# Optimization experiments

Measured on AMD Instinct MI355X. Metric: run time of the kernel, lower is better.

## Reference

```python
import jax, jax.numpy as jnp
import numpy as np

HEADS = 4
DIM_HEAD = 32
DIM = 128
EPS = 1e-12  # F.normalize eps


def _rmsnorm(t, g):
    # F.normalize over channel dim (dim=1), then * g * sqrt(dim)
    n = jnp.sqrt(jnp.sum(t * t, axis=1, keepdims=True))
    return t / jnp.maximum(n, EPS) * g * (DIM ** 0.5)


def setup_inputs() -> dict:
    key = jax.random.key(0)
    ks = jax.random.split(key, 5)
    b, H, W = 16, 96, 96
    x = jax.random.normal(ks[0], (b, DIM, H, W), dtype=jnp.float32)
    norm_g = jnp.ones((1, DIM, 1, 1), dtype=jnp.float32)
    qkv_w = jax.random.normal(ks[1], (3 * HEADS * DIM_HEAD, DIM), dtype=jnp.float32) * 0.05
    mem_kv = jax.random.normal(ks[2], (2, HEADS, DIM_HEAD, 4), dtype=jnp.float32)
    out_w = jax.random.normal(ks[3], (DIM, HEADS * DIM_HEAD), dtype=jnp.float32) * 0.05
    out_b = jnp.zeros((DIM,), dtype=jnp.float32)
    out_norm_g = jnp.ones((1, DIM, 1, 1), dtype=jnp.float32)
    return {"x": x, "norm_g": norm_g, "qkv_w": qkv_w, "mem_kv": mem_kv,
            "out_w": out_w, "out_b": out_b, "out_norm_g": out_norm_g}


def reference(x, norm_g, qkv_w, mem_kv, out_w, out_b, out_norm_g):
    b, c, H, W = x.shape
    n = H * W
    scale = DIM_HEAD ** (-0.5)

    xn = _rmsnorm(x, norm_g)
    # 1x1 conv (no bias) == channel GEMM
    qkv = jnp.einsum('oc,bchw->bohw', qkv_w, xn)  # [b, 3*h*d, H, W]
    q, k, v = jnp.split(qkv, 3, axis=1)

    def to_heads(t):
        return t.reshape(b, HEADS, DIM_HEAD, n)  # b h d n

    q, k, v = to_heads(q), to_heads(k), to_heads(v)

    mk = jnp.broadcast_to(mem_kv[0], (b, HEADS, DIM_HEAD, mem_kv.shape[-1]))
    mv = jnp.broadcast_to(mem_kv[1], (b, HEADS, DIM_HEAD, mem_kv.shape[-1]))
    k = jnp.concatenate([mk, k], axis=-1)
    v = jnp.concatenate([mv, v], axis=-1)

    q = jax.nn.softmax(q, axis=-2) * scale  # softmax over d
    k = jax.nn.softmax(k, axis=-1)          # softmax over n

    context = jnp.einsum('bhdn,bhen->bhde', k, v)  # [b,h,d,d]
    out = jnp.einsum('bhde,bhdn->bhen', context, q)  # [b,h,d,n]
    out = out.reshape(b, HEADS * DIM_HEAD, H, W)

    out = jnp.einsum('oc,bchw->bohw', out_w, out) + out_b[None, :, None, None]
    return _rmsnorm(out, out_norm_g)
```

## Files before the change

kernel.cpp:

```cpp
#include <hip/hip_runtime.h>
#include <hip/hip_bf16.h>
#include <math.h>

#define NPIX 9216
#define NBLK 48
#define TPB 6
#define NTILE 288
#define SCALE 0.17677669529663687f
#define SQRT128 11.313708498984761f

typedef __attribute__((ext_vector_type(8))) short short8;
typedef __attribute__((ext_vector_type(4))) float f32x4;

static __device__ __forceinline__ unsigned short f2bf(float f) {
  return __bfloat16_as_ushort(__float2bfloat16(f));
}
static __device__ __forceinline__ float bf2f(unsigned short h) {
  return __bfloat162float(__ushort_as_bfloat16(h));
}


__global__ __launch_bounds__(256) void k_prep2(
    const float* __restrict__ qkv_w, const float* __restrict__ norm_g,
    const float* __restrict__ out_w,
    unsigned short* __restrict__ wbf2, unsigned short* __restrict__ owb2) {
  const int i = blockIdx.x * 256 + threadIdx.x;
  if (i < 6144) {
    const int g = i >> 6, lane = i & 63;
    const int wv = g / 24, rem = g % 24;
    const int mt = rem >> 2, ks = rem & 3;
    const int row = 96 * wv + mt * 16 + (lane & 15);
    const int col = ks * 32 + (lane >> 4) * 8;
    const float* src = qkv_w + row * 128 + col;
    const float* gg = norm_g + col;
    uint4 o;
    o.x = (unsigned)f2bf(src[0] * gg[0]) | ((unsigned)f2bf(src[1] * gg[1]) << 16);
    o.y = (unsigned)f2bf(src[2] * gg[2]) | ((unsigned)f2bf(src[3] * gg[3]) << 16);
    o.z = (unsigned)f2bf(src[4] * gg[4]) | ((unsigned)f2bf(src[5] * gg[5]) << 16);
    o.w = (unsigned)f2bf(src[6] * gg[6]) | ((unsigned)f2bf(src[7] * gg[7]) << 16);
    *(uint4*)(wbf2 + (size_t)i * 8) = o;
  } else if (i < 8192) {
    const int i2 = i - 6144;
    const int g = i2 >> 6, lane = i2 & 63;
    const int wv = g >> 3, rem = g & 7;
    const int mt = rem >> 2, ks = rem & 3;
    const int row = 32 * wv + mt * 16 + (lane & 15);
    const int col = ks * 32 + (lane >> 4) * 8;
    const float* src = out_w + row * 128 + col;
    uint4 o;
    o.x = (unsigned)f2bf(src[0]) | ((unsigned)f2bf(src[1]) << 16);
    o.y = (unsigned)f2bf(src[2]) | ((unsigned)f2bf(src[3]) << 16);
    o.z = (unsigned)f2bf(src[4]) | ((unsigned)f2bf(src[5]) << 16);
    o.w = (unsigned)f2bf(src[6]) | ((unsigned)f2bf(src[7]) << 16);
    *(uint4*)(owb2 + (size_t)i2 * 8) = o;
  }
}

__global__ __launch_bounds__(256) void k_init(const float* __restrict__ mem_kv,
                                              float* __restrict__ ctxG,
                                              float* __restrict__ sumexpG) {
  const int bh = blockIdx.x;
  const int h = bh & 3;
  const float* mk = mem_kv + h * 128;
  const float* mv = mem_kv + 512 + h * 128;
  const int t = threadIdx.x;
  const int d = t >> 3, e0 = (t & 7) * 4;
  float ek[4], se = 0.f;
#pragma unroll
  for (int j = 0; j < 4; ++j) { ek[j] = __expf(mk[d * 4 + j]); se += ek[j]; }
#pragma unroll
  for (int ei = 0; ei < 4; ++ei) {
    const int e = e0 + ei;
    float s = 0.f;
#pragma unroll
    for (int j = 0; j < 4; ++j) s += ek[j] * mv[e * 4 + j];
    ctxG[(bh * 32 + d) * 32 + e] = s;
  }
  if ((t & 7) == 0) sumexpG[bh * 32 + d] = se;
}

template <bool WSQ>
__global__ __launch_bounds__(256, 2) void k1(
    const float* __restrict__ x, const unsigned short* __restrict__ wbf2,
    unsigned short* __restrict__ qb16, float* __restrict__ qf32,
    float* __restrict__ ctx_dst, float* __restrict__ se_dst) {
  __shared__ __align__(16) unsigned char smem[30720 + 8704 + 4096 + 128];
  unsigned short* qkv = (unsigned short*)smem;
  unsigned short* xnT = (unsigned short*)(smem + 30720);
  float* redu = (float*)(smem + 30720 + 8704);
  float* inv = (float*)(smem + 30720 + 8704 + 4096);

  const int t = threadIdx.x;
  const int b = blockIdx.y;
  const int blk = blockIdx.x;
  const int wv = t >> 6;
  const int lane = t & 63;
  const int lr = lane & 15;
  const int lg = lane >> 4;
  const int r = t >> 3, c4 = (t & 7) * 4;
  const float* xb = x + ((size_t)b * 128) * NPIX + blk * TPB * 32;

  f32x4 acc[6][2];
  f32x4 ctx[2][2];
#pragma unroll
  for (int i = 0; i < 6; ++i)
#pragma unroll
    for (int j = 0; j < 2; ++j)
#pragma unroll
      for (int q = 0; q < 4; ++q) acc[i][j][q] = 0.f;
#pragma unroll
  for (int i = 0; i < 2; ++i)
#pragma unroll
    for (int j = 0; j < 2; ++j)
#pragma unroll
      for (int q = 0; q < 4; ++q) ctx[i][j][q] = 0.f;
  float se_row[2] = {0.f, 0.f};

  float4 pf[4];
#pragma unroll
  for (int pass = 0; pass < 4; ++pass)
    pf[pass] = *(const float4*)(xb + (size_t)(pass * 32 + r) * NPIX + c4);

  for (int it = 0; it < TPB; ++it) {
    const int tile = blk * TPB + it;

    {
      float ss0 = 0.f, ss1 = 0.f, ss2 = 0.f, ss3 = 0.f;
#pragma unroll
      for (int pass = 0; pass < 4; ++pass) {
        const int row = pass * 32 + r;
        const float4 v = pf[pass];
        xnT[(c4 + 0) * 136 + row] = f2bf(v.x);
        xnT[(c4 + 1) * 136 + row] = f2bf(v.y);
        xnT[(c4 + 2) * 136 + row] = f2bf(v.z);
        xnT[(c4 + 3) * 136 + row] = f2bf(v.w);
        ss0 = fmaf(v.x, v.x, ss0); ss1 = fmaf(v.y, v.y, ss1);
        ss2 = fmaf(v.z, v.z, ss2); ss3 = fmaf(v.w, v.w, ss3);
      }
      *(float4*)&redu[r * 32 + c4] = make_float4(ss0, ss1, ss2, ss3);
    }
    __syncthreads();
    {
      short8 bfr[4][2];
#pragma unroll
      for (int ks = 0; ks < 4; ++ks)
#pragma unroll
        for (int nt = 0; nt < 2; ++nt)
          bfr[ks][nt] = *(const short8*)&xnT[(nt * 16 + lr) * 136 + ks * 32 + lg * 8];
      if (it + 1 < TPB) {
        const float* xb2 = xb + (it + 1) * 32;
#pragma unroll
        for (int pass = 0; pass < 4; ++pass)
          pf[pass] = *(const float4*)(xb2 + (size_t)(pass * 32 + r) * NPIX + c4);
      }
      if (t < 32) {
        float s = 0.f;
#pragma unroll
        for (int g = 0; g < 32; ++g) s += redu[g * 32 + t];
        inv[t] = SQRT128 / fmaxf(sqrtf(s), 1e-12f);
      }
      const unsigned short* wbase = wbf2 + (size_t)(wv * 24) * 512 + lane * 8;
#pragma unroll
      for (int mt = 0; mt < 6; ++mt) {
#pragma unroll
        for (int ks = 0; ks < 4; ++ks) {
          const short8 af = *(const short8*)(wbase + (size_t)(mt * 4 + ks) * 512);
          acc[mt][0] = __builtin_amdgcn_mfma_f32_16x16x32_bf16(af, bfr[ks][0], acc[mt][0], 0, 0, 0);
          acc[mt][1] = __builtin_amdgcn_mfma_f32_16x16x32_bf16(af, bfr[ks][1], acc[mt][1], 0, 0, 0);
        }
      }
    }
    __syncthreads();
    {
      const float iv0 = inv[lr], iv1 = inv[16 + lr];
#pragma unroll
      for (int mt = 0; mt < 6; ++mt)
#pragma unroll
        for (int nt = 0; nt < 2; ++nt) {
          const float iv = nt ? iv1 : iv0;
#pragma unroll
          for (int q = 0; q < 4; ++q) {
            const int row = 96 * wv + mt * 16 + lg * 4 + q;
            qkv[row * 40 + nt * 16 + lr] = f2bf(acc[mt][nt][q] * iv);
            acc[mt][nt][q] = 0.f;
          }
        }
    }
    __syncthreads();
    {
      const int c0 = wv * 32 + lg * 8;
#pragma unroll
      for (int px = 0; px < 2; ++px) {
        const int p = px * 16 + lr;
        float qv[8];
#pragma unroll
        for (int j = 0; j < 8; ++j) qv[j] = bf2f(qkv[(c0 + j) * 40 + p]);
        float m = qv[0];
#pragma unroll
        for (int j = 1; j < 8; ++j) m = fmaxf(m, qv[j]);
        m = fmaxf(m, __shfl_xor(m, 16));
        m = fmaxf(m, __shfl_xor(m, 32));
        float s = 0.f;
#pragma unroll
        for (int j = 0; j < 8; ++j) { qv[j] = __expf(qv[j] - m); s += qv[j]; }
        s += __shfl_xor(s, 16);
        s += __shfl_xor(s, 32);
        const float rs = SCALE / s;
        if (WSQ) {
          uint4 qo;
          qo.x = (unsigned)f2bf(qv[0] * rs) | ((unsigned)f2bf(qv[1] * rs) << 16);
          qo.y = (unsigned)f2bf(qv[2] * rs) | ((unsigned)f2bf(qv[3] * rs) << 16);
          qo.z = (unsigned)f2bf(qv[4] * rs) | ((unsigned)f2bf(qv[5] * rs) << 16);
          qo.w = (unsigned)f2bf(qv[6] * rs) | ((unsigned)f2bf(qv[7] * rs) << 16);
          *(uint4*)(qb16 +
              ((((size_t)(b * NTILE + tile) * 4 + wv) * 2 + px) * 64 + lane) * 8) = qo;
        } else {
#pragma unroll
          for (int j = 0; j < 8; ++j)
            qf32[((size_t)b * 128 + c0 + j) * NPIX + tile * 32 + p] = qv[j] * rs;
        }
      }
      short8 afk[2];
#pragma unroll
      for (int dt = 0; dt < 2; ++dt) {
        const short8 kraw = *(const short8*)&qkv[(128 + wv * 32 + dt * 16 + lr) * 40 + lg * 8];
        short8 e16;
        float s = 0.f;
#pragma unroll
        for (int j = 0; j < 8; ++j) {
          const float ev = __expf(bf2f((unsigned short)kraw[j]));
          e16[j] = (short)f2bf(ev);
          s += ev;
        }
        afk[dt] = e16;
        s += __shfl_xor(s, 16);
        s += __shfl_xor(s, 32);
        se_row[dt] += s;
      }
#pragma unroll
      for (int dt = 0; dt < 2; ++dt)
#pragma unroll
        for (int et = 0; et < 2; ++et) {
          const short8 bf = *(const short8*)&qkv[(256 + wv * 32 + et * 16 + lr) * 40 + lg * 8];
          ctx[dt][et] = __builtin_amdgcn_mfma_f32_16x16x32_bf16(afk[dt], bf, ctx[dt][et], 0, 0, 0);
        }
    }
  }

  if (WSQ) {
    float* dst = ctx_dst + ((size_t)(b * NBLK + blk)) * 4096 + wv * 1024;
#pragma unroll
    for (int dt = 0; dt < 2; ++dt)
#pragma unroll
      for (int et = 0; et < 2; ++et)
#pragma unroll
        for (int q = 0; q < 4; ++q)
          dst[(dt * 16 + lg * 4 + q) * 32 + et * 16 + lr] = ctx[dt][et][q];
    if (lg == 0) {
#pragma unroll
      for (int dt = 0; dt < 2; ++dt)
        se_dst[(b * NBLK + blk) * 128 + wv * 32 + dt * 16 + lr] = se_row[dt];
    }
  } else {
#pragma unroll
    for (int dt = 0; dt < 2; ++dt)
#pragma unroll
      for (int et = 0; et < 2; ++et)
#pragma unroll
        for (int q = 0; q < 4; ++q)
          atomicAdd(&ctx_dst[((size_t)b * 128 + wv * 32 + dt * 16 + lg * 4 + q) * 32 + et * 16 + lr],
                    ctx[dt][et][q]);
    if (lg == 0) {
#pragma unroll
      for (int dt = 0; dt < 2; ++dt)
        atomicAdd(&se_dst[b * 128 + wv * 32 + dt * 16 + lr], se_row[dt]);
    }
  }
}

__global__ __launch_bounds__(256) void k_reduce(
    const float* __restrict__ part_ctx, const float* __restrict__ part_se,
    const float* __restrict__ mem_kv, unsigned short* __restrict__ ctxnT) {
  const int bid = blockIdx.x;
  const int b = bid >> 4, h = (bid >> 2) & 3, dq = bid & 3;
  const int t = threadIdx.x;
  const int dd = t >> 5;
  const int d = dq * 8 + dd;
  const int e = t & 31;
  __shared__ float sise[8];

  const float* mk = mem_kv + h * 128 + d * 4;
  const float* mv = mem_kv + 512 + h * 128 + e * 4;
  float ek[4];
  float acc = 0.f;
#pragma unroll
  for (int j = 0; j < 4; ++j) ek[j] = __expf(mk[j]);
#pragma unroll
  for (int j = 0; j < 4; ++j) acc += ek[j] * mv[j];
  const float* src = part_ctx + (size_t)b * NBLK * 4096 + h * 1024 + d * 32 + e;
  for (int p = 0; p < NBLK; ++p) acc += src[(size_t)p * 4096];
  if (e == 0) {
    float se = ek[0] + ek[1] + ek[2] + ek[3];
    const float* sp = part_se + (size_t)b * NBLK * 128 + h * 32 + d;
    for (int p = 0; p < NBLK; ++p) se += sp[(size_t)p * 128];
    sise[dd] = 1.f / se;
  }
  __syncthreads();
  ctxnT[(size_t)(b * 4 + h) * 1024 + e * 32 + d] = f2bf(acc * sise[dd]);
}

__global__ __launch_bounds__(256) void k_norm(
    const float* __restrict__ ctxG, const float* __restrict__ seG,
    unsigned short* __restrict__ ctxnT) {
  const int b = blockIdx.x;
  const int t = threadIdx.x;
  const int h = t >> 6, d = (t >> 1) & 31, e0 = (t & 1) * 16;
  const int r = h * 32 + d;
  const float ise = 1.f / seG[b * 128 + r];
  const float* src = ctxG + ((size_t)b * 128 + r) * 32;
  unsigned short* dst = ctxnT + ((size_t)(b * 4 + h) * 32) * 32;
#pragma unroll
  for (int i = 0; i < 16; ++i)
    dst[(e0 + i) * 32 + d] = f2bf(src[e0 + i] * ise);
}

__global__ __launch_bounds__(256) void k3_ws(
    const unsigned short* __restrict__ ctxnT, const unsigned short* __restrict__ owb2,
    const unsigned short* __restrict__ qbf, const float* __restrict__ out_b,
    const float* __restrict__ out_norm_g, float* __restrict__ out) {
  __shared__ __align__(16) unsigned char smem[8704 + 2048 + 128];
  unsigned short* o1T = (unsigned short*)smem;
  float* redu = (float*)(smem + 8704);
  float* inv = (float*)(smem + 8704 + 2048);

  const int t = threadIdx.x;
  const int b = blockIdx.y;
  const int tile = blockIdx.x;
  const int p0 = tile * 32;
  const int wv = t >> 6;
  const int lane = t & 63;
  const int lr = lane & 15;
  const int lg = lane >> 4;

  {
    f32x4 o1a[2][2];
#pragma unroll
    for (int i = 0; i < 2; ++i)
#pragma unroll
      for (int j = 0; j < 2; ++j)
#pragma unroll
        for (int q = 0; q < 4; ++q) o1a[i][j][q] = 0.f;
    const unsigned short* cbase = ctxnT + (size_t)(b * 4 + wv) * 1024;
    const unsigned short* qb = qbf + (((size_t)(b * NTILE + tile) * 4 + wv) * 2) * 512;
    short8 bq[2];
#pragma unroll
    for (int nt = 0; nt < 2; ++nt)
      bq[nt] = *(const short8*)(qb + (size_t)(nt * 64 + lane) * 8);
#pragma unroll
    for (int mt = 0; mt < 2; ++mt) {
      const short8 af = *(const short8*)(cbase + (mt * 16 + lr) * 32 + lg * 8);
#pragma unroll
      for (int nt = 0; nt < 2; ++nt)
        o1a[mt][nt] = __builtin_amdgcn_mfma_f32_16x16x32_bf16(af, bq[nt], o1a[mt][nt], 0, 0, 0);
    }
#pragma unroll
    for (int mt = 0; mt < 2; ++mt)
#pragma unroll
      for (int nt = 0; nt < 2; ++nt)
#pragma unroll
        for (int q = 0; q < 4; ++q) {
          const int e = wv * 32 + mt * 16 + lg * 4 + q;
          o1T[(nt * 16 + lr) * 136 + e] = f2bf(o1a[mt][nt][q]);
        }
  }
  __syncthreads();
  f32x4 y[2][2];
#pragma unroll
  for (int i = 0; i < 2; ++i)
#pragma unroll
    for (int j = 0; j < 2; ++j)
#pragma unroll
      for (int q = 0; q < 4; ++q) y[i][j][q] = 0.f;
  const unsigned short* wbase = owb2 + (size_t)(wv * 8) * 512 + lane * 8;
#pragma unroll
  for (int mt = 0; mt < 2; ++mt) {
#pragma unroll
    for (int ks = 0; ks < 4; ++ks) {
      const short8 af = *(const short8*)(wbase + (size_t)(mt * 4 + ks) * 512);
#pragma unroll
      for (int nt = 0; nt < 2; ++nt) {
        const short8 bf = *(const short8*)&o1T[(nt * 16 + lr) * 136 + ks * 32 + lg * 8];
        y[mt][nt] = __builtin_amdgcn_mfma_f32_16x16x32_bf16(af, bf, y[mt][nt], 0, 0, 0);
      }
    }
  }
  {
    float ss[2] = {0.f, 0.f};
#pragma unroll
    for (int mt = 0; mt < 2; ++mt)
#pragma unroll
      for (int q = 0; q < 4; ++q) {
        const int row = 32 * wv + mt * 16 + lg * 4 + q;
        const float bb = out_b[row];
#pragma unroll
        for (int nt = 0; nt < 2; ++nt) {
          y[mt][nt][q] += bb;
          ss[nt] = fmaf(y[mt][nt][q], y[mt][nt][q], ss[nt]);
        }
      }
#pragma unroll
    for (int nt = 0; nt < 2; ++nt)
      redu[(wv * 4 + lg) * 32 + nt * 16 + lr] = ss[nt];
  }
  __syncthreads();
  if (t < 32) {
    float s = 0.f;
#pragma unroll
    for (int g = 0; g < 16; ++g) s += redu[g * 32 + t];
    inv[t] = SQRT128 / fmaxf(sqrtf(s), 1e-12f);
  }
  __syncthreads();
  {
    float* ob = out + (size_t)b * 128 * NPIX + p0;
#pragma unroll
    for (int mt = 0; mt < 2; ++mt)
#pragma unroll
      for (int q = 0; q < 4; ++q) {
        const int row = 32 * wv + mt * 16 + lg * 4 + q;
        const float g = out_norm_g[row];
#pragma unroll
        for (int nt = 0; nt < 2; ++nt) {
          const int col = nt * 16 + lr;
          ob[(size_t)row * NPIX + col] = y[mt][nt][q] * inv[col] * g;
        }
      }
  }
}

__global__ __launch_bounds__(256) void k3f(
    const unsigned short* __restrict__ ctxnT, const unsigned short* __restrict__ owb2,
    const float* __restrict__ out_b, const float* __restrict__ out_norm_g,
    float* __restrict__ io) {
  __shared__ __align__(16) unsigned char smem[8704 + 8704 + 2048 + 128];
  unsigned short* qT = (unsigned short*)smem;
  unsigned short* o1T = (unsigned short*)(smem + 8704);
  float* redu = (float*)(smem + 8704 + 8704);
  float* inv = (float*)(smem + 8704 + 8704 + 2048);

  const int t = threadIdx.x;
  const int b = blockIdx.y;
  const int p0 = blockIdx.x * 32;
  const int wv = t >> 6;
  const int lane = t & 63;
  const int lr = lane & 15;
  const int lg = lane >> 4;

  {
    const float* qb = io + (size_t)b * 128 * NPIX + p0;
    const int r = t >> 3, c4 = (t & 7) * 4;
#pragma unroll
    for (int pass = 0; pass < 4; ++pass) {
      const int row = pass * 32 + r;
      const float4 v = *(const float4*)(qb + (size_t)row * NPIX + c4);
      qT[(c4 + 0) * 136 + row] = f2bf(v.x);
      qT[(c4 + 1) * 136 + row] = f2bf(v.y);
      qT[(c4 + 2) * 136 + row] = f2bf(v.z);
      qT[(c4 + 3) * 136 + row] = f2bf(v.w);
    }
  }
  __syncthreads();
  {
    f32x4 o1a[2][2];
#pragma unroll
    for (int i = 0; i < 2; ++i)
#pragma unroll
      for (int j = 0; j < 2; ++j)
#pragma unroll
        for (int q = 0; q < 4; ++q) o1a[i][j][q] = 0.f;
    const unsigned short* cbase = ctxnT + (size_t)(b * 4 + wv) * 1024;
#pragma unroll
    for (int mt = 0; mt < 2; ++mt) {
      const short8 af = *(const short8*)(cbase + (mt * 16 + lr) * 32 + lg * 8);
#pragma unroll
      for (int nt = 0; nt < 2; ++nt) {
        const short8 bf = *(const short8*)&qT[(nt * 16 + lr) * 136 + wv * 32 + lg * 8];
        o1a[mt][nt] = __builtin_amdgcn_mfma_f32_16x16x32_bf16(af, bf, o1a[mt][nt], 0, 0, 0);
      }
    }
#pragma unroll
    for (int mt = 0; mt < 2; ++mt)
#pragma unroll
      for (int nt = 0; nt < 2; ++nt)
#pragma unroll
        for (int q = 0; q < 4; ++q) {
          const int e = wv * 32 + mt * 16 + lg * 4 + q;
          o1T[(nt * 16 + lr) * 136 + e] = f2bf(o1a[mt][nt][q]);
        }
  }
  __syncthreads();
  f32x4 y[2][2];
#pragma unroll
  for (int i = 0; i < 2; ++i)
#pragma unroll
    for (int j = 0; j < 2; ++j)
#pragma unroll
      for (int q = 0; q < 4; ++q) y[i][j][q] = 0.f;
  const unsigned short* wbase = owb2 + (size_t)(wv * 8) * 512 + lane * 8;
#pragma unroll
  for (int mt = 0; mt < 2; ++mt) {
#pragma unroll
    for (int ks = 0; ks < 4; ++ks) {
      const short8 af = *(const short8*)(wbase + (size_t)(mt * 4 + ks) * 512);
#pragma unroll
      for (int nt = 0; nt < 2; ++nt) {
        const short8 bf = *(const short8*)&o1T[(nt * 16 + lr) * 136 + ks * 32 + lg * 8];
        y[mt][nt] = __builtin_amdgcn_mfma_f32_16x16x32_bf16(af, bf, y[mt][nt], 0, 0, 0);
      }
    }
  }
  {
    float ss[2] = {0.f, 0.f};
#pragma unroll
    for (int mt = 0; mt < 2; ++mt)
#pragma unroll
      for (int q = 0; q < 4; ++q) {
        const int row = 32 * wv + mt * 16 + lg * 4 + q;
        const float bb = out_b[row];
#pragma unroll
        for (int nt = 0; nt < 2; ++nt) {
          y[mt][nt][q] += bb;
          ss[nt] = fmaf(y[mt][nt][q], y[mt][nt][q], ss[nt]);
        }
      }
#pragma unroll
    for (int nt = 0; nt < 2; ++nt)
      redu[(wv * 4 + lg) * 32 + nt * 16 + lr] = ss[nt];
  }
  __syncthreads();
  if (t < 32) {
    float s = 0.f;
#pragma unroll
    for (int g = 0; g < 16; ++g) s += redu[g * 32 + t];
    inv[t] = SQRT128 / fmaxf(sqrtf(s), 1e-12f);
  }
  __syncthreads();
  {
    float* ob = io + (size_t)b * 128 * NPIX + p0;
#pragma unroll
    for (int mt = 0; mt < 2; ++mt)
#pragma unroll
      for (int q = 0; q < 4; ++q) {
        const int row = 32 * wv + mt * 16 + lg * 4 + q;
        const float g = out_norm_g[row];
#pragma unroll
        for (int nt = 0; nt < 2; ++nt) {
          const int col = nt * 16 + lr;
          ob[(size_t)row * NPIX + col] = y[mt][nt][q] * inv[col] * g;
        }
      }
  }
}

extern "C" void kernel_launch(void* const* d_in, const int* in_sizes, int n_in,
                              void* d_out, int out_size, void* d_ws, size_t ws_size,
                              hipStream_t stream) {
  const float* x          = (const float*)d_in[0];
  const float* norm_g     = (const float*)d_in[1];
  const float* qkv_w      = (const float*)d_in[2];
  const float* mem_kv     = (const float*)d_in[3];
  const float* out_w      = (const float*)d_in[4];
  const float* out_b      = (const float*)d_in[5];
  const float* out_norm_g = (const float*)d_in[6];
  float* out = (float*)d_out;

  const size_t PC = (size_t)16 * NBLK * 4096;
  const size_t PS = (size_t)16 * NBLK * 128;
  const size_t QB = (size_t)16 * NPIX * 128;
  const size_t need = (PC + PS) * 4 + (49152 + 16384 + 65536 + QB) * 2;

  if (ws_size >= need) {
    float* part_ctx = (float*)d_ws;
    float* part_se  = part_ctx + PC;
    unsigned short* wbf2  = (unsigned short*)(part_se + PS);
    unsigned short* owb2  = wbf2 + 49152;
    unsigned short* ctxnT = owb2 + 16384;
    unsigned short* qbf   = ctxnT + 65536;
    k_prep2<<<32, 256, 0, stream>>>(qkv_w, norm_g, out_w, wbf2, owb2);
    k1<true><<<dim3(NBLK, 16), 256, 0, stream>>>(x, wbf2, qbf, nullptr, part_ctx, part_se);
    k_reduce<<<256, 256, 0, stream>>>(part_ctx, part_se, mem_kv, ctxnT);
    k3_ws<<<dim3(NTILE, 16), 256, 0, stream>>>(ctxnT, owb2, qbf, out_b, out_norm_g, out);
  } else {
    float* ctxG = (float*)d_ws;
    float* seG  = ctxG + 65536;
    unsigned short* wbf2  = (unsigned short*)(seG + 2048);
    unsigned short* owb2  = wbf2 + 49152;
    unsigned short* ctxnT = owb2 + 16384;
    k_prep2<<<32, 256, 0, stream>>>(qkv_w, norm_g, out_w, wbf2, owb2);
    k_init<<<64, 256, 0, stream>>>(mem_kv, ctxG, seG);
    k1<false><<<dim3(NBLK, 16), 256, 0, stream>>>(x, wbf2, nullptr, out, ctxG, seG);
    k_norm<<<16, 256, 0, stream>>>(ctxG, seG, ctxnT);
    k3f<<<dim3(NTILE, 16), 256, 0, stream>>>(ctxnT, owb2, out_b, out_norm_g, out);
  }
}
```

Baseline: 77.42 us.

## Reorder QKV weights per head so each wave owns its q/k/v rows, drop barriers

The packed QKV weight layout is permuted so each wave's 96 output rows are the q, k and v rows of its own head. This lets each wave write and read a private slice of the qkv shared buffer, which removes two of the three block-wide barriers per tile. The xnT and reduction buffers are double-buffered to avoid write-after-read hazards across iterations. The sum-of-squares reduction is pre-folded with a shuffle and every wave now computes the inverse norms itself, replacing the single-thread-group computation that needed a barrier. This uses more shared memory, and correctness relies on wave-level ordering of LDS accesses without explicit barriers.

```diff
diff --git a/kernel.cpp b/kernel.cpp
--- a/kernel.cpp
+++ b/kernel.cpp
@@ -29,7 +29,7 @@
     const int g = i >> 6, lane = i & 63;
     const int wv = g / 24, rem = g % 24;
     const int mt = rem >> 2, ks = rem & 3;
-    const int row = 96 * wv + mt * 16 + (lane & 15);
+    const int row = (mt >> 1) * 128 + wv * 32 + (mt & 1) * 16 + (lane & 15);
     const int col = ks * 32 + (lane >> 4) * 8;
     const float* src = qkv_w + row * 128 + col;
     const float* gg = norm_g + col;
@@ -84,11 +84,10 @@
     const float* __restrict__ x, const unsigned short* __restrict__ wbf2,
     unsigned short* __restrict__ qb16, float* __restrict__ qf32,
     float* __restrict__ ctx_dst, float* __restrict__ se_dst) {
-  __shared__ __align__(16) unsigned char smem[30720 + 8704 + 4096 + 128];
+  __shared__ __align__(16) unsigned char smem[30720 + 17408 + 4096];
   unsigned short* qkv = (unsigned short*)smem;
-  unsigned short* xnT = (unsigned short*)(smem + 30720);
-  float* redu = (float*)(smem + 30720 + 8704);
-  float* inv = (float*)(smem + 30720 + 8704 + 4096);
+  unsigned short* xnT0 = (unsigned short*)(smem + 30720);
+  float* redu0 = (float*)(smem + 30720 + 17408);
 
   const int t = threadIdx.x;
   const int b = blockIdx.y;
@@ -99,6 +98,7 @@
   const int lg = lane >> 4;
   const int r = t >> 3, c4 = (t & 7) * 4;
   const float* xb = x + ((size_t)b * 128) * NPIX + blk * TPB * 32;
+  unsigned short* qkv_w = qkv + wv * 96 * 40;
 
   f32x4 acc[6][2];
   f32x4 ctx[2][2];
@@ -123,6 +123,8 @@
 
   for (int it = 0; it < TPB; ++it) {
     const int tile = blk * TPB + it;
+    unsigned short* xnT = xnT0 + (it & 1) * 4352;
+    float* redu = redu0 + (it & 1) * 512;
 
     {
       float ss0 = 0.f, ss1 = 0.f, ss2 = 0.f, ss3 = 0.f;
@@ -137,9 +139,24 @@
         ss0 = fmaf(v.x, v.x, ss0); ss1 = fmaf(v.y, v.y, ss1);
         ss2 = fmaf(v.z, v.z, ss2); ss3 = fmaf(v.w, v.w, ss3);
       }
-      *(float4*)&redu[r * 32 + c4] = make_float4(ss0, ss1, ss2, ss3);
+      ss0 += __shfl_xor(ss0, 8); ss1 += __shfl_xor(ss1, 8);
+      ss2 += __shfl_xor(ss2, 8); ss3 += __shfl_xor(ss3, 8);
+      if (!(t & 8))
+        *(float4*)&redu[(t >> 4) * 32 + c4] = make_float4(ss0, ss1, ss2, ss3);
     }
     __syncthreads();
+    float iv0, iv1;
+    {
+      float invv = 0.f;
+      if (lane < 32) {
+        float s = 0.f;
+#pragma unroll
+        for (int g = 0; g < 16; ++g) s += redu[g * 32 + lane];
+        invv = SQRT128 / fmaxf(sqrtf(s), 1e-12f);
+      }
+      iv0 = __shfl(invv, lr);
+      iv1 = __shfl(invv, 16 + lr);
+    }
     {
       short8 bfr[4][2];
 #pragma unroll
@@ -153,12 +170,6 @@
         for (int pass = 0; pass < 4; ++pass)
           pf[pass] = *(const float4*)(xb2 + (size_t)(pass * 32 + r) * NPIX + c4);
       }
-      if (t < 32) {
-        float s = 0.f;
-#pragma unroll
-        for (int g = 0; g < 32; ++g) s += redu[g * 32 + t];
-        inv[t] = SQRT128 / fmaxf(sqrtf(s), 1e-12f);
-      }
       const unsigned short* wbase = wbf2 + (size_t)(wv * 24) * 512 + lane * 8;
 #pragma unroll
       for (int mt = 0; mt < 6; ++mt) {
@@ -170,9 +181,7 @@
         }
       }
     }
-    __syncthreads();
     {
-      const float iv0 = inv[lr], iv1 = inv[16 + lr];
 #pragma unroll
       for (int mt = 0; mt < 6; ++mt)
 #pragma unroll
@@ -180,21 +189,19 @@
           const float iv = nt ? iv1 : iv0;
 #pragma unroll
           for (int q = 0; q < 4; ++q) {
-            const int row = 96 * wv + mt * 16 + lg * 4 + q;
-            qkv[row * 40 + nt * 16 + lr] = f2bf(acc[mt][nt][q] * iv);
+            const int row_l = mt * 16 + lg * 4 + q;
+            qkv_w[row_l * 40 + nt * 16 + lr] = f2bf(acc[mt][nt][q] * iv);
             acc[mt][nt][q] = 0.f;
           }
         }
     }
-    __syncthreads();
     {
-      const int c0 = wv * 32 + lg * 8;
 #pragma unroll
       for (int px = 0; px < 2; ++px) {
         const int p = px * 16 + lr;
         float qv[8];
 #pragma unroll
-        for (int j = 0; j < 8; ++j) qv[j] = bf2f(qkv[(c0 + j) * 40 + p]);
+        for (int j = 0; j < 8; ++j) qv[j] = bf2f(qkv_w[(lg * 8 + j) * 40 + p]);
         float m = qv[0];
 #pragma unroll
         for (int j = 1; j < 8; ++j) m = fmaxf(m, qv[j]);
@@ -215,15 +222,16 @@
           *(uint4*)(qb16 +
               ((((size_t)(b * NTILE + tile) * 4 + wv) * 2 + px) * 64 + lane) * 8) = qo;
         } else {
+          const int c0g = wv * 32 + lg * 8;
 #pragma unroll
           for (int j = 0; j < 8; ++j)
-            qf32[((size_t)b * 128 + c0 + j) * NPIX + tile * 32 + p] = qv[j] * rs;
+            qf32[((size_t)b * 128 + c0g + j) * NPIX + tile * 32 + p] = qv[j] * rs;
         }
       }
       short8 afk[2];
 #pragma unroll
       for (int dt = 0; dt < 2; ++dt) {
-        const short8 kraw = *(const short8*)&qkv[(128 + wv * 32 + dt * 16 + lr) * 40 + lg * 8];
+        const short8 kraw = *(const short8*)&qkv_w[(32 + dt * 16 + lr) * 40 + lg * 8];
         short8 e16;
         float s = 0.f;
 #pragma unroll
@@ -241,7 +249,7 @@
       for (int dt = 0; dt < 2; ++dt)
 #pragma unroll
         for (int et = 0; et < 2; ++et) {
-          const short8 bf = *(const short8*)&qkv[(256 + wv * 32 + et * 16 + lr) * 40 + lg * 8];
+          const short8 bf = *(const short8*)&qkv_w[(64 + et * 16 + lr) * 40 + lg * 8];
           ctx[dt][et] = __builtin_amdgcn_mfma_f32_16x16x32_bf16(afk[dt], bf, ctx[dt][et], 0, 0, 0);
         }
     }
```

Measured after the change: 76.02 us. About the same (-1.8%).
